# Optimization experiments

Hardware: AMD Instinct MI355X
Metric: run time of the kernel (lower is better)

Reference implementation:

```python
import jax, jax.numpy as jnp
import numpy as np

T, C, N, H = 60, 128, 4096, 128  # timesteps, channels(=hidden), pixel samples, hidden
GP = 5  # gp_affected_timesteps


def setup_inputs() -> dict:
    key = jax.random.key(0)
    k1, k2, k3 = jax.random.split(key, 3)
    s = 1.0 / np.sqrt(H)
    return {
        "image_stack": jax.random.normal(k1, (T, C, N), dtype=jnp.float32),
        "mask": jnp.zeros((T, N), dtype=jnp.float32),  # accepted but unused by original forward
        "W_ih": jax.random.uniform(k2, (4 * H, C), dtype=jnp.float32, minval=-s, maxval=s),
        "W_hh": jax.random.uniform(k3, (4 * H, H), dtype=jnp.float32, minval=-s, maxval=s),
        "b_ih": jnp.zeros((4 * H,), dtype=jnp.float32),
        "b_hh": jnp.zeros((4 * H,), dtype=jnp.float32),
        "gp_affected_timesteps": GP,
    }


def _lstm_cell(carry, xt, W_ih, W_hh, b):
    h, c = carry
    gates = xt @ W_ih.T + h @ W_hh.T + b  # [N, 4H]
    i, f, g, o = jnp.split(gates, 4, axis=-1)
    i, f, o = jax.nn.sigmoid(i), jax.nn.sigmoid(f), jax.nn.sigmoid(o)
    g = jnp.tanh(g)
    c = f * c + i * g
    h = o * jnp.tanh(c)
    return (h, c), h


def reference(image_stack, mask, W_ih, W_hh, b_ih, b_hh, gp_affected_timesteps):
    t, ch, n = image_stack.shape
    h = ch  # output fed back as input => hidden == channels
    b = b_ih + b_hh
    xs = jnp.transpose(image_stack, (0, 2, 1))  # [T, N, C]
    init = (jnp.zeros((n, h), image_stack.dtype), jnp.zeros((n, h), image_stack.dtype))

    cell = lambda carry, xt: _lstm_cell(carry, xt, W_ih, W_hh, b)
    carry, outs1 = jax.lax.scan(cell, init, xs)  # [T, N, H]

    extra = t - gp_affected_timesteps - 1
    ar = lambda carry, _: _lstm_cell(carry, carry[0], W_ih, W_hh, b)
    carry, outs2 = jax.lax.scan(ar, carry, None, length=extra)  # [extra, N, H]

    outs = jnp.concatenate([outs1, outs2], axis=0)  # [T+extra, N, H]
    return jnp.transpose(outs, (1, 0, 2))  # batch-first [N, T+extra, H]
```

## Files before the change

kernel.cpp:

```cpp
#include <hip/hip_runtime.h>
#include <hip/hip_bf16.h>

typedef __attribute__((ext_vector_type(8))) short short8;
typedef __attribute__((ext_vector_type(4))) float f32x4;

constexpr int T    = 60;
constexpr int C    = 128;
constexpr int NPIX = 4096;
constexpr int H    = 128;
constexpr int GP   = 5;
constexpr int EXTRA = T - GP - 1;
constexpr int TT    = T + EXTRA;
constexpr int LDS_STRIDE = 136;

__device__ __forceinline__ unsigned short f2bf(float f) {
  unsigned u = __float_as_uint(f);
  u += 0x7FFF + ((u >> 16) & 1);
  return (unsigned short)(u >> 16);
}
__device__ __forceinline__ float bf2f(unsigned short s) {
  return __uint_as_float(((unsigned)s) << 16);
}
__device__ __forceinline__ float fast_sigmoid(float x) {
  float e = __builtin_amdgcn_exp2f(-1.44269504f * x);
  return __builtin_amdgcn_rcpf(1.0f + e);
}
__device__ __forceinline__ float fast_tanh(float x) {
  float e = __builtin_amdgcn_exp2f(2.88539008f * x);
  return 1.0f - 2.0f * __builtin_amdgcn_rcpf(1.0f + e);
}

__global__ __launch_bounds__(512, 2) void lstm_persistent(
    const float* __restrict__ img,
    const float* __restrict__ wih,
    const float* __restrict__ whh,
    const float* __restrict__ bih,
    const float* __restrict__ bhh,
    float* __restrict__ out)
{
  __shared__ __align__(16) unsigned short xs[16 * LDS_STRIDE];
  __shared__ __align__(16) unsigned short hs[16 * LDS_STRIDE];

  const int tid  = threadIdx.x;
  const int lane = tid & 63;
  const int w    = tid >> 6;
  const int l15  = lane & 15;
  const int quad = lane >> 4;
  const int n0   = blockIdx.x * 16;
  const int hid  = w * 16 + l15;

  short8 fih[4][4], fhh[4][4];
  float bias[4];
  #pragma unroll
  for (int nt = 0; nt < 4; ++nt) {
    const int col = nt * 128 + hid;
    bias[nt] = bih[col] + bhh[col];
    #pragma unroll
    for (int kt = 0; kt < 4; ++kt) {
      const int k0 = kt * 32 + quad * 8;
      const float* pih = wih + col * C + k0;
      const float* phh = whh + col * C + k0;
      short8 a, b;
      #pragma unroll
      for (int j = 0; j < 8; ++j) {
        a[j] = (short)f2bf(pih[j]);
        b[j] = (short)f2bf(phh[j]);
      }
      fih[nt][kt] = a;
      fhh[nt][kt] = b;
    }
  }

  for (int i = tid; i < 16 * LDS_STRIDE; i += 512) hs[i] = 0;

  float c[4] = {0.f, 0.f, 0.f, 0.f};

  const int nl = tid & 15;
  const int cb = (tid >> 4) * 4;
  const float* xbase = img + (size_t)cb * NPIX + n0 + nl;

  {
    float p0 = xbase[0], p1 = xbase[NPIX], p2 = xbase[2 * NPIX], p3 = xbase[3 * NPIX];
    ushort4 pk;
    pk.x = f2bf(p0); pk.y = f2bf(p1); pk.z = f2bf(p2); pk.w = f2bf(p3);
    *(ushort4*)&xs[nl * LDS_STRIDE + cb] = pk;
  }
  __syncthreads();

  const int fro = l15 * LDS_STRIDE + quad * 8;

  for (int t = 0; t < TT; ++t) {
    const bool pf = (t + 1 < T);
    float q0, q1, q2, q3;
    if (pf) {
      const float* p = xbase + (size_t)(t + 1) * C * NPIX;
      q0 = p[0]; q1 = p[NPIX]; q2 = p[2 * NPIX]; q3 = p[3 * NPIX];
    }

    if (t == T) {
      #pragma unroll
      for (int nt = 0; nt < 4; ++nt)
        #pragma unroll
        for (int kt = 0; kt < 4; ++kt) {
          short8 a = fih[nt][kt], b = fhh[nt][kt];
          #pragma unroll
          for (int j = 0; j < 8; ++j)
            a[j] = (short)f2bf(bf2f((unsigned short)a[j]) + bf2f((unsigned short)b[j]));
          fih[nt][kt] = a;
        }
    }

    f32x4 acc[4];
    #pragma unroll
    for (int nt = 0; nt < 4; ++nt)
      acc[nt] = (f32x4){bias[nt], bias[nt], bias[nt], bias[nt]};

    if (t < T) {
      #pragma unroll
      for (int kt = 0; kt < 4; ++kt) {
        short8 ax = *(const short8*)&xs[fro + kt * 32];
        short8 ah = *(const short8*)&hs[fro + kt * 32];
        #pragma unroll
        for (int nt = 0; nt < 4; ++nt) {
          acc[nt] = __builtin_amdgcn_mfma_f32_16x16x32_bf16(ax, fih[nt][kt], acc[nt], 0, 0, 0);
          acc[nt] = __builtin_amdgcn_mfma_f32_16x16x32_bf16(ah, fhh[nt][kt], acc[nt], 0, 0, 0);
        }
      }
    } else {
      #pragma unroll
      for (int kt = 0; kt < 4; ++kt) {
        short8 ah = *(const short8*)&hs[fro + kt * 32];
        #pragma unroll
        for (int nt = 0; nt < 4; ++nt)
          acc[nt] = __builtin_amdgcn_mfma_f32_16x16x32_bf16(ah, fih[nt][kt], acc[nt], 0, 0, 0);
      }
    }

    float hv[4];
    #pragma unroll
    for (int r = 0; r < 4; ++r) {
      float ig = fast_sigmoid(acc[0][r]);
      float fg = fast_sigmoid(acc[1][r]);
      float gg = fast_tanh(acc[2][r]);
      float og = fast_sigmoid(acc[3][r]);
      c[r] = fg * c[r] + ig * gg;
      hv[r] = og * fast_tanh(c[r]);
    }

    {
      float* ob = out + (size_t)(n0 + quad * 4) * (TT * H) + (size_t)t * H + hid;
      #pragma unroll
      for (int r = 0; r < 4; ++r)
        __builtin_nontemporal_store(hv[r], ob + (size_t)r * (TT * H));
    }

    __syncthreads();

    if (pf) {
      ushort4 pk;
      pk.x = f2bf(q0); pk.y = f2bf(q1); pk.z = f2bf(q2); pk.w = f2bf(q3);
      *(ushort4*)&xs[nl * LDS_STRIDE + cb] = pk;
    }
    #pragma unroll
    for (int r = 0; r < 4; ++r)
      hs[(quad * 4 + r) * LDS_STRIDE + hid] = f2bf(hv[r]);

    __syncthreads();
  }
}

extern "C" void kernel_launch(void* const* d_in, const int* in_sizes, int n_in,
                              void* d_out, int out_size, void* d_ws, size_t ws_size,
                              hipStream_t stream) {
  (void)in_sizes; (void)n_in; (void)d_ws; (void)ws_size; (void)out_size;
  const float* img = (const float*)d_in[0];
  const float* wih = (const float*)d_in[2];
  const float* whh = (const float*)d_in[3];
  const float* bih = (const float*)d_in[4];
  const float* bhh = (const float*)d_in[5];
  float* out = (float*)d_out;

  lstm_persistent<<<NPIX / 16, 512, 0, stream>>>(img, wih, whh, bih, bhh, out);
}
```

Before: 425.2 us.

## Double-buffer LDS state, split recurrence loops, defer output stores

Double-buffers the x and h tiles in LDS so each timestep needs one barrier instead of two. The time loop is split into a teacher-forced phase and an autoregressive phase, which removes per-step branches and moves the weight merge out of the loop. Each step's output stores are deferred to the start of the next step so they overlap with compute. The x prefetch now uses a float4 load along pixels with scattered 2-byte LDS writes, which may add bank conflicts in exchange for fewer global load instructions.

```diff
diff --git a/kernel.cpp b/kernel.cpp
--- a/kernel.cpp
+++ b/kernel.cpp
@@ -11,7 +11,7 @@
 constexpr int GP   = 5;
 constexpr int EXTRA = T - GP - 1;
 constexpr int TT    = T + EXTRA;
-constexpr int LDS_STRIDE = 136;
+constexpr int LS    = 136;
 
 __device__ __forceinline__ unsigned short f2bf(float f) {
   unsigned u = __float_as_uint(f);
@@ -38,8 +38,8 @@
     const float* __restrict__ bhh,
     float* __restrict__ out)
 {
-  __shared__ __align__(16) unsigned short xs[16 * LDS_STRIDE];
-  __shared__ __align__(16) unsigned short hs[16 * LDS_STRIDE];
+  __shared__ __align__(16) unsigned short xs[2][16 * LS];
+  __shared__ __align__(16) unsigned short hs[2][16 * LS];
 
   const int tid  = threadIdx.x;
   const int lane = tid & 63;
@@ -71,102 +71,130 @@
     }
   }
 
-  for (int i = tid; i < 16 * LDS_STRIDE; i += 512) hs[i] = 0;
-
-  float c[4] = {0.f, 0.f, 0.f, 0.f};
-
-  const int nl = tid & 15;
-  const int cb = (tid >> 4) * 4;
-  const float* xbase = img + (size_t)cb * NPIX + n0 + nl;
-
+  const int xc = tid >> 2;
+  const int xn = (tid & 3) * 4;
+  const float* xptr = img + (size_t)xc * NPIX + n0 + xn;
   {
-    float p0 = xbase[0], p1 = xbase[NPIX], p2 = xbase[2 * NPIX], p3 = xbase[3 * NPIX];
-    ushort4 pk;
-    pk.x = f2bf(p0); pk.y = f2bf(p1); pk.z = f2bf(p2); pk.w = f2bf(p3);
-    *(ushort4*)&xs[nl * LDS_STRIDE + cb] = pk;
-  }
+    float4 v = *(const float4*)xptr;
+    xs[0][(xn + 0) * LS + xc] = f2bf(v.x);
+    xs[0][(xn + 1) * LS + xc] = f2bf(v.y);
+    xs[0][(xn + 2) * LS + xc] = f2bf(v.z);
+    xs[0][(xn + 3) * LS + xc] = f2bf(v.w);
+  }
+  for (int i = tid; i < 16 * LS; i += 512) hs[0][i] = 0;
   __syncthreads();
 
-  const int fro = l15 * LDS_STRIDE + quad * 8;
-
-  for (int t = 0; t < TT; ++t) {
+  float cc[4] = {0.f, 0.f, 0.f, 0.f};
+  float hv[4];
+  const int fro = l15 * LS + quad * 8;
+
+  float* ob = out + (size_t)(n0 + quad * 4) * (TT * H) + hid;
+  const size_t ostep = (size_t)TT * H;
+  const float* xpf = xptr + (size_t)C * NPIX;
+
+  for (int t = 0; t < T; ++t) {
+    const int rb = t & 1, wb = rb ^ 1;
+
+    if (t > 0) {
+      #pragma unroll
+      for (int r = 0; r < 4; ++r)
+        __builtin_nontemporal_store(hv[r], ob + (size_t)r * ostep);
+      ob += H;
+    }
+
     const bool pf = (t + 1 < T);
-    float q0, q1, q2, q3;
-    if (pf) {
-      const float* p = xbase + (size_t)(t + 1) * C * NPIX;
-      q0 = p[0]; q1 = p[NPIX]; q2 = p[2 * NPIX]; q3 = p[3 * NPIX];
-    }
-
-    if (t == T) {
-      #pragma unroll
-      for (int nt = 0; nt < 4; ++nt)
-        #pragma unroll
-        for (int kt = 0; kt < 4; ++kt) {
-          short8 a = fih[nt][kt], b = fhh[nt][kt];
-          #pragma unroll
-          for (int j = 0; j < 8; ++j)
-            a[j] = (short)f2bf(bf2f((unsigned short)a[j]) + bf2f((unsigned short)b[j]));
-          fih[nt][kt] = a;
-        }
-    }
+    float4 q;
+    if (pf) { q = *(const float4*)xpf; xpf += (size_t)C * NPIX; }
 
     f32x4 acc[4];
     #pragma unroll
     for (int nt = 0; nt < 4; ++nt)
       acc[nt] = (f32x4){bias[nt], bias[nt], bias[nt], bias[nt]};
 
-    if (t < T) {
-      #pragma unroll
-      for (int kt = 0; kt < 4; ++kt) {
-        short8 ax = *(const short8*)&xs[fro + kt * 32];
-        short8 ah = *(const short8*)&hs[fro + kt * 32];
-        #pragma unroll
-        for (int nt = 0; nt < 4; ++nt) {
-          acc[nt] = __builtin_amdgcn_mfma_f32_16x16x32_bf16(ax, fih[nt][kt], acc[nt], 0, 0, 0);
-          acc[nt] = __builtin_amdgcn_mfma_f32_16x16x32_bf16(ah, fhh[nt][kt], acc[nt], 0, 0, 0);
-        }
+    #pragma unroll
+    for (int kt = 0; kt < 4; ++kt) {
+      short8 ax = *(const short8*)&xs[rb][fro + kt * 32];
+      short8 ah = *(const short8*)&hs[rb][fro + kt * 32];
+      #pragma unroll
+      for (int nt = 0; nt < 4; ++nt) {
+        acc[nt] = __builtin_amdgcn_mfma_f32_16x16x32_bf16(ax, fih[nt][kt], acc[nt], 0, 0, 0);
+        acc[nt] = __builtin_amdgcn_mfma_f32_16x16x32_bf16(ah, fhh[nt][kt], acc[nt], 0, 0, 0);
       }
-    } else {
-      #pragma unroll
-      for (int kt = 0; kt < 4; ++kt) {
-        short8 ah = *(const short8*)&hs[fro + kt * 32];
-        #pragma unroll
-        for (int nt = 0; nt < 4; ++nt)
-          acc[nt] = __builtin_amdgcn_mfma_f32_16x16x32_bf16(ah, fih[nt][kt], acc[nt], 0, 0, 0);
-      }
-    }
-
-    float hv[4];
+    }
+
     #pragma unroll
     for (int r = 0; r < 4; ++r) {
       float ig = fast_sigmoid(acc[0][r]);
       float fg = fast_sigmoid(acc[1][r]);
       float gg = fast_tanh(acc[2][r]);
       float og = fast_sigmoid(acc[3][r]);
-      c[r] = fg * c[r] + ig * gg;
-      hv[r] = og * fast_tanh(c[r]);
-    }
-
-    {
-      float* ob = out + (size_t)(n0 + quad * 4) * (TT * H) + (size_t)t * H + hid;
-      #pragma unroll
-      for (int r = 0; r < 4; ++r)
-        __builtin_nontemporal_store(hv[r], ob + (size_t)r * (TT * H));
-    }
-
+      cc[r] = fg * cc[r] + ig * gg;
+      hv[r] = og * fast_tanh(cc[r]);
+    }
+
+    #pragma unroll
+    for (int r = 0; r < 4; ++r)
+      hs[wb][(quad * 4 + r) * LS + hid] = f2bf(hv[r]);
+    if (pf) {
+      xs[wb][(xn + 0) * LS + xc] = f2bf(q.x);
+      xs[wb][(xn + 1) * LS + xc] = f2bf(q.y);
+      xs[wb][(xn + 2) * LS + xc] = f2bf(q.z);
+      xs[wb][(xn + 3) * LS + xc] = f2bf(q.w);
+    }
     __syncthreads();
-
-    if (pf) {
-      ushort4 pk;
-      pk.x = f2bf(q0); pk.y = f2bf(q1); pk.z = f2bf(q2); pk.w = f2bf(q3);
-      *(ushort4*)&xs[nl * LDS_STRIDE + cb] = pk;
-    }
+  }
+
+  #pragma unroll
+  for (int nt = 0; nt < 4; ++nt)
+    #pragma unroll
+    for (int kt = 0; kt < 4; ++kt) {
+      short8 a = fih[nt][kt], b = fhh[nt][kt];
+      #pragma unroll
+      for (int j = 0; j < 8; ++j)
+        a[j] = (short)f2bf(bf2f((unsigned short)a[j]) + bf2f((unsigned short)b[j]));
+      fih[nt][kt] = a;
+    }
+
+  for (int t = T; t < TT; ++t) {
+    const int rb = t & 1, wb = rb ^ 1;
+
     #pragma unroll
     for (int r = 0; r < 4; ++r)
-      hs[(quad * 4 + r) * LDS_STRIDE + hid] = f2bf(hv[r]);
-
+      __builtin_nontemporal_store(hv[r], ob + (size_t)r * ostep);
+    ob += H;
+
+    f32x4 acc[4];
+    #pragma unroll
+    for (int nt = 0; nt < 4; ++nt)
+      acc[nt] = (f32x4){bias[nt], bias[nt], bias[nt], bias[nt]};
+
+    #pragma unroll
+    for (int kt = 0; kt < 4; ++kt) {
+      short8 ah = *(const short8*)&hs[rb][fro + kt * 32];
+      #pragma unroll
+      for (int nt = 0; nt < 4; ++nt)
+        acc[nt] = __builtin_amdgcn_mfma_f32_16x16x32_bf16(ah, fih[nt][kt], acc[nt], 0, 0, 0);
+    }
+
+    #pragma unroll
+    for (int r = 0; r < 4; ++r) {
+      float ig = fast_sigmoid(acc[0][r]);
+      float fg = fast_sigmoid(acc[1][r]);
+      float gg = fast_tanh(acc[2][r]);
+      float og = fast_sigmoid(acc[3][r]);
+      cc[r] = fg * cc[r] + ig * gg;
+      hv[r] = og * fast_tanh(cc[r]);
+    }
+
+    #pragma unroll
+    for (int r = 0; r < 4; ++r)
+      hs[wb][(quad * 4 + r) * LS + hid] = f2bf(hv[r]);
     __syncthreads();
   }
+
+  #pragma unroll
+  for (int r = 0; r < 4; ++r)
+    __builtin_nontemporal_store(hv[r], ob + (size_t)r * ostep);
 }
 
 extern "C" void kernel_launch(void* const* d_in, const int* in_sizes, int n_in,
```

Result: slower. 522.5 us (+22.9%).
